# Optimization experiments

Measured on AMD Instinct MI355X. Metric: run time of the kernel, lower is better.

Reference implementation:

```python
import jax, jax.numpy as jnp
import numpy as np

N_NODES = 100000
N_EDGES = 800000
NODE_F = 32
EDGE_F = 16
HID = 128
EPS = 1e-5


def _bn(h, g, b):
    # BatchNorm1d in training mode: biased batch stats over dim 0
    m = h.mean(axis=0)
    v = jnp.mean((h - m) ** 2, axis=0)
    return (h - m) * jax.lax.rsqrt(v + EPS) * g + b


def _sage(x, src, dst, Wl, bl, Wr):
    # PyG SAGEConv (mean aggr): lin_l(mean_{j->i} x_j) + lin_r(x_i)
    s = jax.ops.segment_sum(x[src], dst, num_segments=N_NODES)
    cnt = jax.ops.segment_sum(jnp.ones((src.shape[0], 1), x.dtype), dst, num_segments=N_NODES)
    mean = s / jnp.maximum(cnt, 1.0)
    return mean @ Wl + bl + x @ Wr


def setup_inputs() -> dict:
    key = jax.random.key(0)
    ks = jax.random.split(key, 32)

    def lin(k, fi, fo):
        return jax.random.normal(k, (fi, fo), jnp.float32) / np.sqrt(fi)

    inp = {
        'x': jax.random.normal(ks[0], (N_NODES, NODE_F), jnp.float32),
        'edge_index': jax.random.randint(ks[1], (2, N_EDGES), 0, N_NODES),
        'edge_attr': jax.random.normal(ks[2], (N_EDGES, EDGE_F), jnp.float32),
        'edge_source': jax.random.randint(ks[3], (N_EDGES,), 0, N_NODES),
        'edge_target': jax.random.randint(ks[4], (N_EDGES,), 0, N_NODES),
        'W1l': lin(ks[5], NODE_F, HID), 'b1': jnp.zeros((HID,), jnp.float32), 'W1r': lin(ks[6], NODE_F, HID),
        'W2l': lin(ks[7], HID, HID), 'b2': jnp.zeros((HID,), jnp.float32), 'W2r': lin(ks[8], HID, HID),
        'bn1_g': jnp.ones((HID,), jnp.float32), 'bn1_b': jnp.zeros((HID,), jnp.float32),
        'bn2_g': jnp.ones((HID,), jnp.float32), 'bn2_b': jnp.zeros((HID,), jnp.float32),
        'We': lin(ks[9], EDGE_F, HID), 'be': jnp.zeros((HID,), jnp.float32),
        'bne_g': jnp.ones((HID,), jnp.float32), 'bne_b': jnp.zeros((HID,), jnp.float32),
        'Wm1': lin(ks[10], 3 * HID, HID), 'bm1': jnp.zeros((HID,), jnp.float32),
        'bnm_g': jnp.ones((HID,), jnp.float32), 'bnm_b': jnp.zeros((HID,), jnp.float32),
        'Wm2': lin(ks[11], HID, HID // 2), 'bm2': jnp.zeros((HID // 2,), jnp.float32),
        'Wm3': lin(ks[12], HID // 2, 1), 'bm3': jnp.zeros((1,), jnp.float32),
    }
    return inp


def reference(x, edge_index, edge_attr, edge_source, edge_target,
              W1l, b1, W1r, W2l, b2, W2r, bn1_g, bn1_b, bn2_g, bn2_b,
              We, be, bne_g, bne_b, Wm1, bm1, bnm_g, bnm_b, Wm2, bm2, Wm3, bm3):
    src, dst = edge_index[0], edge_index[1]
    h = jax.nn.relu(_bn(_sage(x, src, dst, W1l, b1, W1r), bn1_g, bn1_b))  # dropout = identity (eval)
    h = jax.nn.relu(_bn(_sage(h, src, dst, W2l, b2, W2r), bn2_g, bn2_b))
    ef = _bn(jax.nn.relu(edge_attr @ We + be), bne_g, bne_b)  # Linear->ReLU->BN->Dropout(id)
    z = jnp.concatenate([h[edge_source], h[edge_target], ef], axis=1)  # [E, 3*HID]
    z = _bn(jax.nn.relu(z @ Wm1 + bm1), bnm_g, bnm_b)
    z = jax.nn.relu(z @ Wm2 + bm2)
    return (z @ Wm3 + bm3).squeeze(-1)
```

## Files before the change

kernel.cpp:

```cpp
#include <hip/hip_runtime.h>
#include <hip/hip_bf16.h>

#define NN 100000
#define NE 800000
#define SCAN_NB 98

typedef __attribute__((ext_vector_type(8))) short bf16x8;
typedef __attribute__((ext_vector_type(4))) float f32x4;

__device__ __forceinline__ short f2b(float f) {
    unsigned u = __float_as_uint(f);
    unsigned r = (u + 0x7fffu + ((u >> 16) & 1u)) >> 16;
    return (short)r;
}
__device__ __forceinline__ float b2f(short s) {
    return __uint_as_float(((unsigned)(unsigned short)s) << 16);
}

__global__ __launch_bounds__(256) void k_hist(const int* __restrict__ ei, int* __restrict__ deg)
{
    int e = blockIdx.x * 256 + threadIdx.x;
    if (e < NE) atomicAdd(&deg[ei[NE + e]], 1);
}

__global__ __launch_bounds__(1024) void k_scan_a(const int* __restrict__ deg,
    int* __restrict__ tmp, int* __restrict__ bsum)
{
    __shared__ int sh[1024];
    int t = threadIdx.x, b = blockIdx.x;
    int idx = b * 1024 + t;
    int v = (idx < NN) ? deg[idx] : 0;
    sh[t] = v;
    __syncthreads();
    for (int ofs = 1; ofs < 1024; ofs <<= 1) {
        int u = (t >= ofs) ? sh[t - ofs] : 0;
        __syncthreads();
        sh[t] += u;
        __syncthreads();
    }
    if (idx < NN) tmp[idx] = sh[t] - v;
    if (t == 1023) bsum[b] = sh[1023];
}

__global__ void k_scan_b(const int* __restrict__ bsum, int* __restrict__ boff,
    int* __restrict__ rowptr)
{
    if (threadIdx.x == 0) {
        int acc = 0;
        for (int i = 0; i < SCAN_NB; i++) { boff[i] = acc; acc += bsum[i]; }
        rowptr[NN] = acc;
    }
}

__global__ __launch_bounds__(1024) void k_scan_c(const int* __restrict__ tmp,
    const int* __restrict__ boff, int* __restrict__ rowptr, int* __restrict__ wp)
{
    int b = blockIdx.x, t = threadIdx.x;
    int idx = b * 1024 + t;
    if (idx < NN) {
        int v = boff[b] + tmp[idx];
        rowptr[idx] = v; wp[idx] = v;
    }
}

__global__ __launch_bounds__(256) void k_scatter(const int* __restrict__ ei,
    int* __restrict__ wp, int* __restrict__ elist)
{
    int e = blockIdx.x * 256 + threadIdx.x;
    if (e < NE) {
        int d = ei[NE + e];
        int pos = atomicAdd(&wp[d], 1);
        elist[pos] = ei[e];
    }
}

__global__ __launch_bounds__(256) void k_gagg1(const float* __restrict__ x,
    const int* __restrict__ rowptr, const int* __restrict__ elist, float* __restrict__ meanX)
{
    int n = blockIdx.x * 8 + (threadIdx.x >> 5);
    int j = threadIdx.x & 31;
    int b = rowptr[n], e = rowptr[n + 1];
    float acc = 0.f;
    for (int i = b; i < e; i++) {
        int s = elist[i];
        acc += x[(size_t)s * 32 + j];
    }
    float inv = (e > b) ? 1.0f / (float)(e - b) : 1.0f;
    meanX[(size_t)n * 32 + j] = acc * inv;
}

__global__ __launch_bounds__(256) void k_gagg2(const short* __restrict__ h1b,
    const int* __restrict__ rowptr, const int* __restrict__ elist,
    const float* __restrict__ sc1, const float* __restrict__ sh1, short* __restrict__ m2b)
{
    int n = blockIdx.x * 8 + (threadIdx.x >> 5);
    int c0 = (threadIdx.x & 31) * 4;
    float sc[4], sh[4];
    #pragma unroll
    for (int i = 0; i < 4; i++) { sc[i] = sc1[c0 + i]; sh[i] = sh1[c0 + i]; }
    int b = rowptr[n], e = rowptr[n + 1];
    float acc[4] = {0.f, 0.f, 0.f, 0.f};
    for (int i = b; i < e; i++) {
        int s = elist[i];
        ushort4 u = *(const ushort4*)(h1b + (size_t)s * 128 + c0);
        acc[0] += fmaxf(b2f((short)u.x) * sc[0] + sh[0], 0.f);
        acc[1] += fmaxf(b2f((short)u.y) * sc[1] + sh[1], 0.f);
        acc[2] += fmaxf(b2f((short)u.z) * sc[2] + sh[2], 0.f);
        acc[3] += fmaxf(b2f((short)u.w) * sc[3] + sh[3], 0.f);
    }
    float inv = (e > b) ? 1.0f / (float)(e - b) : 1.0f;
    ushort4 o;
    o.x = (unsigned short)f2b(acc[0] * inv);
    o.y = (unsigned short)f2b(acc[1] * inv);
    o.z = (unsigned short)f2b(acc[2] * inv);
    o.w = (unsigned short)f2b(acc[3] * inv);
    *(ushort4*)(m2b + (size_t)n * 128 + c0) = o;
}

__global__ __launch_bounds__(256) void k_node_l1(
    const float* __restrict__ meanX, const float* __restrict__ x,
    const float* __restrict__ Wl, const float* __restrict__ Wr,
    const float* __restrict__ bias,
    short* __restrict__ outp, float* __restrict__ ssum, float* __restrict__ ssq)
{
    __shared__ __align__(16) float sWl[32][128];
    __shared__ __align__(16) float sWr[32][128];
    __shared__ __align__(16) float sA[32][36];
    __shared__ __align__(16) float sB[32][36];
    __shared__ float red[2][128], red2[2][128];
    int tid = threadIdx.x;
    int j = tid & 127, rg = tid >> 7;
    int r0 = blockIdx.x * 32;

    for (int f = tid * 4; f < 4096; f += 1024) {
        *(float4*)((float*)sWl + f) = *(const float4*)(Wl + f);
        *(float4*)((float*)sWr + f) = *(const float4*)(Wr + f);
    }
    {
        int r = tid >> 3, c = (tid & 7) * 4;
        *(float4*)(&sA[r][c]) = *(const float4*)(meanX + (size_t)(r0 + r) * 32 + c);
        *(float4*)(&sB[r][c]) = *(const float4*)(x + (size_t)(r0 + r) * 32 + c);
    }
    __syncthreads();

    float acc[16];
    #pragma unroll
    for (int r = 0; r < 16; r++) acc[r] = 0.0f;
    int rb = rg * 16;
    #pragma unroll
    for (int kq = 0; kq < 8; kq++) {
        int k = kq * 4;
        float wl0 = sWl[k][j], wl1 = sWl[k+1][j], wl2 = sWl[k+2][j], wl3 = sWl[k+3][j];
        float wr0 = sWr[k][j], wr1 = sWr[k+1][j], wr2 = sWr[k+2][j], wr3 = sWr[k+3][j];
        #pragma unroll
        for (int r = 0; r < 16; r++) {
            float4 a = *(float4*)(&sA[rb + r][k]);
            float4 b = *(float4*)(&sB[rb + r][k]);
            acc[r] += a.x*wl0 + a.y*wl1 + a.z*wl2 + a.w*wl3
                    + b.x*wr0 + b.y*wr1 + b.z*wr2 + b.w*wr3;
        }
    }
    float bj = bias[j];
    float s1 = 0.0f, s2 = 0.0f;
    #pragma unroll
    for (int r = 0; r < 16; r++) {
        float v = acc[r] + bj;
        outp[(size_t)(r0 + rb + r) * 128 + j] = f2b(v);
        s1 += v; s2 += v * v;
    }
    red[rg][j] = s1; red2[rg][j] = s2;
    __syncthreads();
    if (rg == 0) {
        atomicAdd(&ssum[j], red[0][j] + red[1][j]);
        atomicAdd(&ssq[j],  red2[0][j] + red2[1][j]);
    }
}

__global__ __launch_bounds__(256) void k_node_l2m(
    const short* __restrict__ m2b, const short* __restrict__ h1b,
    const float* __restrict__ sc1, const float* __restrict__ sh1,
    const short* __restrict__ W2cT, const float* __restrict__ bias,
    short* __restrict__ h2b, float* __restrict__ ssum, float* __restrict__ ssq)
{
    __shared__ __align__(16) short sK[32][264];
    __shared__ float sRed[2][128];
    __shared__ float sS[128], sH[128];
    const int tid = threadIdx.x;
    const int wave = tid >> 6, lane = tid & 63, quad = lane >> 4, ln = lane & 15;
    const int waveM = wave >> 1, waveN = wave & 1;
    const int colbase = 64 * waveN, row16 = 16 * waveM;
    if (tid < 128) { sS[tid] = sc1[tid]; sH[tid] = sh1[tid]; sRed[0][tid] = 0.f; sRed[1][tid] = 0.f; }

    bf16x8 bW[4][8];
    #pragma unroll
    for (int nt = 0; nt < 4; nt++)
        #pragma unroll
        for (int kk = 0; kk < 8; kk++)
            bW[nt][kk] = *(const bf16x8*)(W2cT + (size_t)(colbase + nt * 16 + ln) * 256 + kk * 32 + quad * 8);
    float bc[4];
    #pragma unroll
    for (int nt = 0; nt < 4; nt++) bc[nt] = bias[colbase + nt * 16 + ln];

    float s1[4] = {0,0,0,0}, s2[4] = {0,0,0,0};
    f32x4 zero = {0.f, 0.f, 0.f, 0.f};
    __syncthreads();

    for (int t = blockIdx.x; t < NN / 32; t += gridDim.x) {
        int r0 = t * 32;
        __syncthreads();
        {
            int r = tid >> 3, seg = tid & 7;
            if (seg < 4) {
                const bf16x8* src = (const bf16x8*)(m2b + (size_t)(r0 + r) * 128 + seg * 32);
                bf16x8* dst = (bf16x8*)(&sK[r][seg * 32]);
                dst[0] = src[0]; dst[1] = src[1]; dst[2] = src[2]; dst[3] = src[3];
            } else {
                int c0 = (seg - 4) * 32;
                const short* src = h1b + (size_t)(r0 + r) * 128 + c0;
                short tmp[32];
                #pragma unroll
                for (int i = 0; i < 32; i++)
                    tmp[i] = f2b(fmaxf(b2f(src[i]) * sS[c0 + i] + sH[c0 + i], 0.f));
                bf16x8* dst = (bf16x8*)(&sK[r][128 + c0]);
                dst[0] = *(bf16x8*)(tmp); dst[1] = *(bf16x8*)(tmp + 8);
                dst[2] = *(bf16x8*)(tmp + 16); dst[3] = *(bf16x8*)(tmp + 24);
            }
        }
        __syncthreads();
        f32x4 acc[4] = {zero, zero, zero, zero};
        #pragma unroll
        for (int kk = 0; kk < 8; kk++) {
            bf16x8 a = *(const bf16x8*)(&sK[row16 + ln][kk * 32 + quad * 8]);
            #pragma unroll
            for (int nt = 0; nt < 4; nt++)
                acc[nt] = __builtin_amdgcn_mfma_f32_16x16x32_bf16(a, bW[nt][kk], acc[nt], 0, 0, 0);
        }
        #pragma unroll
        for (int nt = 0; nt < 4; nt++) {
            int col = colbase + nt * 16 + ln;
            #pragma unroll
            for (int r = 0; r < 4; r++) {
                float v = acc[nt][r] + bc[nt];
                h2b[(size_t)(r0 + row16 + quad * 4 + r) * 128 + col] = f2b(v);
                s1[nt] += v; s2[nt] += v * v;
            }
        }
    }
    #pragma unroll
    for (int nt = 0; nt < 4; nt++) {
        float a1 = s1[nt], a2 = s2[nt];
        a1 += __shfl_down(a1, 32); a1 += __shfl_down(a1, 16);
        a2 += __shfl_down(a2, 32); a2 += __shfl_down(a2, 16);
        if (quad == 0) {
            atomicAdd(&sRed[0][colbase + nt * 16 + ln], a1);
            atomicAdd(&sRed[1][colbase + nt * 16 + ln], a2);
        }
    }
    __syncthreads();
    if (tid < 128) {
        atomicAdd(&ssum[tid], sRed[0][tid]);
        atomicAdd(&ssq[tid],  sRed[1][tid]);
    }
}

__global__ void k_bn_fin(const float* __restrict__ ssum, const float* __restrict__ ssq,
    const float* __restrict__ g, const float* __restrict__ b, float count,
    float* __restrict__ scale, float* __restrict__ shift)
{
    int j = threadIdx.x;
    float m = ssum[j] / count;
    float var = ssq[j] / count - m * m;
    float rs = rsqrtf(var + 1e-5f);
    float sc = g[j] * rs;
    scale[j] = sc;
    shift[j] = b[j] - m * sc;
}

__global__ void k_prep(const float* __restrict__ We, const float* __restrict__ Wm1,
                       const float* __restrict__ W2l, const float* __restrict__ W2r,
                       short* __restrict__ WteT, short* __restrict__ WmsT,
                       short* __restrict__ WmdT, short* __restrict__ W2cT)
{
    int j = threadIdx.x;
    int b = blockIdx.x;
    if (b == 0) {
        for (int k = 0; k < 32; k++)
            WteT[j * 32 + k] = (k < 16) ? f2b(We[k * 128 + j]) : (short)0;
    } else if (b == 1) {
        for (int k = 0; k < 128; k++) WmsT[j * 128 + k] = f2b(Wm1[k * 128 + j]);
    } else if (b == 2) {
        for (int k = 0; k < 128; k++) WmdT[j * 128 + k] = f2b(Wm1[(128 + k) * 128 + j]);
    } else if (b == 3) {
        for (int k = 0; k < 128; k++) W2cT[j * 256 + k] = f2b(W2l[k * 128 + j]);
    } else {
        for (int k = 0; k < 128; k++) W2cT[j * 256 + 128 + k] = f2b(W2r[k * 128 + j]);
    }
}

__global__ void k_fold_e(const float* __restrict__ ssum, const float* __restrict__ ssq,
    const float* __restrict__ g, const float* __restrict__ b,
    const float* __restrict__ Wm1, const float* __restrict__ bm1,
    short* __restrict__ W1pT, float* __restrict__ bm1p)
{
    __shared__ float sa[128], sc[128];
    int tid = threadIdx.x;
    float m = ssum[tid] / (float)NE;
    float var = ssq[tid] / (float)NE - m * m;
    float rs = rsqrtf(var + 1e-5f);
    float a = g[tid] * rs;
    sa[tid] = a; sc[tid] = b[tid] - m * a;
    __syncthreads();
    float acc = bm1[tid];
    for (int k = 0; k < 128; k++) {
        float w = Wm1[(256 + k) * 128 + tid];
        W1pT[tid * 128 + k] = f2b(sa[k] * w);
        acc += sc[k] * w;
    }
    bm1p[tid] = acc;
}

__global__ void k_fold_m(const float* __restrict__ ssum, const float* __restrict__ ssq,
    const float* __restrict__ g, const float* __restrict__ b,
    const float* __restrict__ Wm2, const float* __restrict__ bm2,
    short* __restrict__ W2pT, float* __restrict__ b2p)
{
    __shared__ float sa[128], sc[128];
    int tid = threadIdx.x;
    float m = ssum[tid] / (float)NE;
    float var = ssq[tid] / (float)NE - m * m;
    float rs = rsqrtf(var + 1e-5f);
    float a = g[tid] * rs;
    sa[tid] = a; sc[tid] = b[tid] - m * a;
    __syncthreads();
    if (tid < 64) {
        float acc = bm2[tid];
        for (int k = 0; k < 128; k++) {
            float w = Wm2[k * 64 + tid];
            W2pT[tid * 128 + k] = f2b(sa[k] * w);
            acc += sc[k] * w;
        }
        b2p[tid] = acc;
    }
}

__global__ __launch_bounds__(256) void k_proj_mfma(
    const short* __restrict__ h2b, const float* __restrict__ sc2, const float* __restrict__ sh2,
    const short* __restrict__ WT, short* __restrict__ C)
{
    __shared__ __align__(16) short sA[32][136];
    __shared__ float sS[128], sH[128];
    const int tid = threadIdx.x;
    const int wave = tid >> 6, lane = tid & 63, quad = lane >> 4, ln = lane & 15;
    const int waveM = wave >> 1, waveN = wave & 1;
    const int colbase = 64 * waveN, row16 = 16 * waveM;
    if (tid < 128) { sS[tid] = sc2[tid]; sH[tid] = sh2[tid]; }
    bf16x8 bW[4][4];
    #pragma unroll
    for (int nt = 0; nt < 4; nt++)
        #pragma unroll
        for (int kk = 0; kk < 4; kk++)
            bW[nt][kk] = *(const bf16x8*)(WT + (colbase + nt * 16 + ln) * 128 + kk * 32 + quad * 8);
    f32x4 zero = {0.f, 0.f, 0.f, 0.f};
    __syncthreads();
    for (int t = blockIdx.x; t < NN / 32; t += gridDim.x) {
        int r0 = t * 32;
        __syncthreads();
        {
            int r = tid >> 3, c0 = (tid & 7) * 16;
            const short* p = h2b + (size_t)(r0 + r) * 128 + c0;
            short tmp[16];
            #pragma unroll
            for (int i = 0; i < 16; i++)
                tmp[i] = f2b(fmaxf(b2f(p[i]) * sS[c0 + i] + sH[c0 + i], 0.f));
            *(bf16x8*)(&sA[r][c0])     = *(bf16x8*)tmp;
            *(bf16x8*)(&sA[r][c0 + 8]) = *(bf16x8*)(tmp + 8);
        }
        __syncthreads();
        f32x4 acc[4] = {zero, zero, zero, zero};
        #pragma unroll
        for (int kk = 0; kk < 4; kk++) {
            bf16x8 a = *(const bf16x8*)(&sA[row16 + ln][kk * 32 + quad * 8]);
            #pragma unroll
            for (int nt = 0; nt < 4; nt++)
                acc[nt] = __builtin_amdgcn_mfma_f32_16x16x32_bf16(a, bW[nt][kk], acc[nt], 0, 0, 0);
        }
        #pragma unroll
        for (int nt = 0; nt < 4; nt++) {
            int col = colbase + nt * 16 + ln;
            #pragma unroll
            for (int r = 0; r < 4; r++)
                C[(size_t)(r0 + row16 + quad * 4 + r) * 128 + col] = f2b(acc[nt][r]);
        }
    }
}

template<int MODE, bool STOREV = false>
__global__ __launch_bounds__(256) void k_edge_mfma(
    const float* __restrict__ ea,
    const short* __restrict__ WteT, const float* __restrict__ be,
    const short* __restrict__ W1pT, const float* __restrict__ bm1p,
    const short* __restrict__ hs, const short* __restrict__ hd,
    const int* __restrict__ esrc, const int* __restrict__ etgt,
    const short* __restrict__ W2pT, const float* __restrict__ b2p,
    const float* __restrict__ Wm3, const float* __restrict__ bm3,
    float* __restrict__ ssum, float* __restrict__ ssq,
    short* __restrict__ vbuf, float* __restrict__ outp)
{
    __shared__ __align__(16) short sT[32][136];
    __shared__ float sRed[2][128];
    __shared__ __align__(16) short sW2[64][136];
    __shared__ float sZ[32][69];
    __shared__ float sW3[64];

    const int tid = threadIdx.x;
    const int wave = tid >> 6, lane = tid & 63;
    const int quad = lane >> 4, ln = lane & 15;
    const int waveM = wave >> 1, waveN = wave & 1;
    const int colbase = 64 * waveN, row16 = 16 * waveM;

    if (MODE < 2) {
        if (tid < 128) { sRed[0][tid] = 0.f; sRed[1][tid] = 0.f; }
    }
    if (MODE >= 2) {
        int q = tid >> 2, kb = (tid & 3) * 32;
        const bf16x8* src = (const bf16x8*)(W2pT + q * 128 + kb);
        bf16x8* dst = (bf16x8*)(&sW2[q][kb]);
        dst[0] = src[0]; dst[1] = src[1]; dst[2] = src[2]; dst[3] = src[3];
        if (tid < 64) sW3[tid] = Wm3[tid];
    }

    bf16x8 bWe[4], bW1[4][4];
    if (MODE <= 2) {
        #pragma unroll
        for (int nt = 0; nt < 4; nt++) {
            bWe[nt] = *(const bf16x8*)(WteT + (colbase + nt * 16 + ln) * 32 + quad * 8);
            if (MODE >= 1) {
                #pragma unroll
                for (int kk = 0; kk < 4; kk++)
                    bW1[nt][kk] = *(const bf16x8*)(W1pT + (colbase + nt * 16 + ln) * 128 + kk * 32 + quad * 8);
            }
        }
    }
    float bec[4], bmc[4];
    #pragma unroll
    for (int nt = 0; nt < 4; nt++) {
        bec[nt] = (MODE <= 2) ? be[colbase + nt * 16 + ln] : 0.f;
        bmc[nt] = (MODE == 1 || MODE == 2) ? bm1p[colbase + nt * 16 + ln] : 0.f;
    }
    float b2c[2] = {0.f, 0.f};
    if (MODE >= 2) { b2c[0] = b2p[32 * waveN + ln]; b2c[1] = b2p[32 * waveN + 16 + ln]; }
    float bm3v = (MODE >= 2) ? bm3[0] : 0.f;

    float s1[4] = {0,0,0,0}, s2[4] = {0,0,0,0};
    f32x4 zero = {0.f, 0.f, 0.f, 0.f};
    __syncthreads();

    for (int t = blockIdx.x; t < NE / 32; t += gridDim.x) {
        const int e0 = t * 32;

        if (MODE == 3) {
            f32x4 vacc[2] = {zero, zero};
            #pragma unroll
            for (int kk = 0; kk < 4; kk++) {
                bf16x8 aV = *(const bf16x8*)(vbuf + (size_t)(e0 + row16 + ln) * 128 + kk * 32 + quad * 8);
                #pragma unroll
                for (int n2 = 0; n2 < 2; n2++) {
                    bf16x8 bV = *(const bf16x8*)(&sW2[32 * waveN + n2 * 16 + ln][kk * 32 + quad * 8]);
                    vacc[n2] = __builtin_amdgcn_mfma_f32_16x16x32_bf16(aV, bV, vacc[n2], 0, 0, 0);
                }
            }
            __syncthreads();
            #pragma unroll
            for (int n2 = 0; n2 < 2; n2++) {
                int col2 = 32 * waveN + n2 * 16 + ln;
                #pragma unroll
                for (int r = 0; r < 4; r++)
                    sZ[row16 + quad * 4 + r][col2] = fmaxf(vacc[n2][r] + b2c[n2], 0.f);
            }
            __syncthreads();
            if (wave == 0) {
                int rw = lane & 31, half = lane >> 5;
                float o = 0.f;
                #pragma unroll 8
                for (int k2 = 0; k2 < 32; k2++)
                    o += sZ[rw][half * 32 + k2] * sW3[half * 32 + k2];
                o += __shfl_down(o, 32);
                if (lane < 32) outp[e0 + rw] = o + bm3v;
            }
            continue;
        }

        bf16x8 aE;
        #pragma unroll
        for (int i = 0; i < 8; i++) aE[i] = 0;
        if (quad < 2) {
            const float* p = ea + (size_t)(e0 + row16 + ln) * 16 + quad * 8;
            float4 f0 = *(const float4*)p, f1 = *(const float4*)(p + 4);
            aE[0]=f2b(f0.x); aE[1]=f2b(f0.y); aE[2]=f2b(f0.z); aE[3]=f2b(f0.w);
            aE[4]=f2b(f1.x); aE[5]=f2b(f1.y); aE[6]=f2b(f1.z); aE[7]=f2b(f1.w);
        }
        f32x4 tacc[4];
        #pragma unroll
        for (int nt = 0; nt < 4; nt++)
            tacc[nt] = __builtin_amdgcn_mfma_f32_16x16x32_bf16(aE, bWe[nt], zero, 0, 0, 0);

        if (MODE == 0) {
            #pragma unroll
            for (int nt = 0; nt < 4; nt++)
                #pragma unroll
                for (int r = 0; r < 4; r++) {
                    float v = fmaxf(tacc[nt][r] + bec[nt], 0.f);
                    s1[nt] += v; s2[nt] += v * v;
                }
            continue;
        }

        __syncthreads();
        #pragma unroll
        for (int nt = 0; nt < 4; nt++) {
            int col = colbase + nt * 16 + ln;
            #pragma unroll
            for (int r = 0; r < 4; r++)
                sT[row16 + quad * 4 + r][col] = f2b(fmaxf(tacc[nt][r] + bec[nt], 0.f));
        }
        __syncthreads();

        f32x4 uacc[4] = {zero, zero, zero, zero};
        #pragma unroll
        for (int kk = 0; kk < 4; kk++) {
            bf16x8 aU = *(const bf16x8*)(&sT[row16 + ln][kk * 32 + quad * 8]);
            #pragma unroll
            for (int nt = 0; nt < 4; nt++)
                uacc[nt] = __builtin_amdgcn_mfma_f32_16x16x32_bf16(aU, bW1[nt][kk], uacc[nt], 0, 0, 0);
        }

        int4 is4 = *(const int4*)(esrc + e0 + row16 + quad * 4);
        int4 it4 = *(const int4*)(etgt + e0 + row16 + quad * 4);
        int isv[4] = {is4.x, is4.y, is4.z, is4.w};
        int itv[4] = {it4.x, it4.y, it4.z, it4.w};

        if (MODE == 1) {
            #pragma unroll
            for (int nt = 0; nt < 4; nt++) {
                int col = colbase + nt * 16 + ln;
                #pragma unroll
                for (int r = 0; r < 4; r++) {
                    float v = uacc[nt][r] + bmc[nt]
                            + b2f(hs[(size_t)isv[r] * 128 + col]) + b2f(hd[(size_t)itv[r] * 128 + col]);
                    v = fmaxf(v, 0.f);
                    s1[nt] += v; s2[nt] += v * v;
                    if constexpr (STOREV)
                        vbuf[(size_t)(e0 + row16 + quad * 4 + r) * 128 + col] = f2b(v);
                }
            }
        } else {
            __syncthreads();
            #pragma unroll
            for (int nt = 0; nt < 4; nt++) {
                int col = colbase + nt * 16 + ln;
                #pragma unroll
                for (int r = 0; r < 4; r++) {
                    float v = uacc[nt][r] + bmc[nt]
                            + b2f(hs[(size_t)isv[r] * 128 + col]) + b2f(hd[(size_t)itv[r] * 128 + col]);
                    sT[row16 + quad * 4 + r][col] = f2b(fmaxf(v, 0.f));
                }
            }
            __syncthreads();
            f32x4 vacc[2] = {zero, zero};
            #pragma unroll
            for (int kk = 0; kk < 4; kk++) {
                bf16x8 aV = *(const bf16x8*)(&sT[row16 + ln][kk * 32 + quad * 8]);
                #pragma unroll
                for (int n2 = 0; n2 < 2; n2++) {
                    bf16x8 bV = *(const bf16x8*)(&sW2[32 * waveN + n2 * 16 + ln][kk * 32 + quad * 8]);
                    vacc[n2] = __builtin_amdgcn_mfma_f32_16x16x32_bf16(aV, bV, vacc[n2], 0, 0, 0);
                }
            }
            #pragma unroll
            for (int n2 = 0; n2 < 2; n2++) {
                int col2 = 32 * waveN + n2 * 16 + ln;
                #pragma unroll
                for (int r = 0; r < 4; r++)
                    sZ[row16 + quad * 4 + r][col2] = fmaxf(vacc[n2][r] + b2c[n2], 0.f);
            }
            __syncthreads();
            if (wave == 0) {
                int rw = lane & 31, half = lane >> 5;
                float o = 0.f;
                #pragma unroll 8
                for (int k2 = 0; k2 < 32; k2++)
                    o += sZ[rw][half * 32 + k2] * sW3[half * 32 + k2];
                o += __shfl_down(o, 32);
                if (lane < 32) outp[e0 + rw] = o + bm3v;
            }
        }
    }

    if (MODE < 2) {
        #pragma unroll
        for (int nt = 0; nt < 4; nt++) {
            float a1 = s1[nt], a2 = s2[nt];
            a1 += __shfl_down(a1, 32); a1 += __shfl_down(a1, 16);
            a2 += __shfl_down(a2, 32); a2 += __shfl_down(a2, 16);
            if (quad == 0) {
                atomicAdd(&sRed[0][colbase + nt * 16 + ln], a1);
                atomicAdd(&sRed[1][colbase + nt * 16 + ln], a2);
            }
        }
        __syncthreads();
        if (tid < 128) {
            atomicAdd(&ssum[tid], sRed[0][tid]);
            atomicAdd(&ssq[tid],  sRed[1][tid]);
        }
    }
}

extern "C" void kernel_launch(void* const* d_in, const int* in_sizes, int n_in,
                              void* d_out, int out_size, void* d_ws, size_t ws_size,
                              hipStream_t stream) {
    const float* x     = (const float*)d_in[0];
    const int*   ei    = (const int*)  d_in[1];
    const float* eattr = (const float*)d_in[2];
    const int*   esrc  = (const int*)  d_in[3];
    const int*   etgt  = (const int*)  d_in[4];
    const float* W1l = (const float*)d_in[5];  const float* b1 = (const float*)d_in[6];
    const float* W1r = (const float*)d_in[7];
    const float* W2l = (const float*)d_in[8];  const float* b2 = (const float*)d_in[9];
    const float* W2r = (const float*)d_in[10];
    const float* bn1_g = (const float*)d_in[11]; const float* bn1_b = (const float*)d_in[12];
    const float* bn2_g = (const float*)d_in[13]; const float* bn2_b = (const float*)d_in[14];
    const float* We  = (const float*)d_in[15]; const float* be  = (const float*)d_in[16];
    const float* bne_g = (const float*)d_in[17]; const float* bne_b = (const float*)d_in[18];
    const float* Wm1 = (const float*)d_in[19]; const float* bm1 = (const float*)d_in[20];
    const float* bnm_g = (const float*)d_in[21]; const float* bnm_b = (const float*)d_in[22];
    const float* Wm2 = (const float*)d_in[23]; const float* bm2 = (const float*)d_in[24];
    const float* Wm3 = (const float*)d_in[25]; const float* bm3 = (const float*)d_in[26];
    float* out = (float*)d_out;

    char* base = (char*)d_ws;
    size_t o = 0;
    auto A = [&](size_t bytes) { char* p = base + o; o = (o + bytes + 255) & ~(size_t)255; return p; };
    short* hsb   = (short*)A((size_t)NN * 128 * 2);
    short* hdb   = (short*)A((size_t)NN * 128 * 2);
    int*   deg   = (int*)  A((size_t)NN * 4);
    int*   rowptr= (int*)  A((size_t)(NN + 1) * 4);
    int*   wp    = (int*)  A((size_t)NN * 4);
    int*   elist = (int*)  A((size_t)NE * 4);
    float* st    = (float*)A(1024 * 4);
    int*   bsum  = (int*)  A(SCAN_NB * 4);
    int*   boff  = (int*)  A(SCAN_NB * 4);
    float* sc1   = (float*)A(512); float* sh1 = (float*)A(512);
    float* sc2   = (float*)A(512); float* sh2 = (float*)A(512);
    float* bm1p  = (float*)A(512); float* b2p = (float*)A(256);
    short* WteT  = (short*)A(128 * 32 * 2);
    short* W1pT  = (short*)A(128 * 128 * 2);
    short* WmsT  = (short*)A(128 * 128 * 2);
    short* WmdT  = (short*)A(128 * 128 * 2);
    short* W2pT  = (short*)A(64 * 128 * 2);
    short* W2cT  = (short*)A(128 * 256 * 2);
    size_t chain = o;
    float* meanX = (float*)A((size_t)NN * 32 * 4);
    short* h1b   = (short*)A((size_t)NN * 128 * 2);
    short* m2b   = (short*)A((size_t)NN * 128 * 2);
    short* h2b   = (short*)A((size_t)NN * 128 * 2);
    int*   stmp  = (int*)meanX;
    short* vbuf  = (short*)(base + chain);
    bool storev = ws_size >= chain + (size_t)NE * 128 * 2;

    hipMemsetAsync(deg, 0, (size_t)NN * 4, stream);
    hipMemsetAsync(st, 0, 1024 * 4, stream);

    k_prep<<<5, 128, 0, stream>>>(We, Wm1, W2l, W2r, WteT, WmsT, WmdT, W2cT);
    k_hist<<<(NE + 255) / 256, 256, 0, stream>>>(ei, deg);
    k_scan_a<<<SCAN_NB, 1024, 0, stream>>>(deg, stmp, bsum);
    k_scan_b<<<1, 64, 0, stream>>>(bsum, boff, rowptr);
    k_scan_c<<<SCAN_NB, 1024, 0, stream>>>(stmp, boff, rowptr, wp);
    k_scatter<<<(NE + 255) / 256, 256, 0, stream>>>(ei, wp, elist);

    k_edge_mfma<0><<<1024, 256, 0, stream>>>(eattr, WteT, be, W1pT, bm1p, hsb, hdb,
        esrc, etgt, W2pT, b2p, Wm3, bm3, st + 512, st + 640, nullptr, out);
    k_fold_e<<<1, 128, 0, stream>>>(st + 512, st + 640, bne_g, bne_b, Wm1, bm1, W1pT, bm1p);

    k_gagg1<<<NN / 8, 256, 0, stream>>>(x, rowptr, elist, meanX);
    k_node_l1<<<NN / 32, 256, 0, stream>>>(meanX, x, W1l, W1r, b1, h1b, st + 0, st + 128);
    k_bn_fin<<<1, 128, 0, stream>>>(st + 0, st + 128, bn1_g, bn1_b, (float)NN, sc1, sh1);

    k_gagg2<<<NN / 8, 256, 0, stream>>>(h1b, rowptr, elist, sc1, sh1, m2b);
    k_node_l2m<<<640, 256, 0, stream>>>(m2b, h1b, sc1, sh1, W2cT, b2, h2b, st + 256, st + 384);
    k_bn_fin<<<1, 128, 0, stream>>>(st + 256, st + 384, bn2_g, bn2_b, (float)NN, sc2, sh2);

    k_proj_mfma<<<640, 256, 0, stream>>>(h2b, sc2, sh2, WmsT, hsb);
    k_proj_mfma<<<640, 256, 0, stream>>>(h2b, sc2, sh2, WmdT, hdb);

    if (storev)
        k_edge_mfma<1, true><<<1280, 256, 0, stream>>>(eattr, WteT, be, W1pT, bm1p, hsb, hdb,
            esrc, etgt, W2pT, b2p, Wm3, bm3, st + 768, st + 896, vbuf, out);
    else
        k_edge_mfma<1, false><<<1280, 256, 0, stream>>>(eattr, WteT, be, W1pT, bm1p, hsb, hdb,
            esrc, etgt, W2pT, b2p, Wm3, bm3, st + 768, st + 896, nullptr, out);
    k_fold_m<<<1, 128, 0, stream>>>(st + 768, st + 896, bnm_g, bnm_b, Wm2, bm2, W2pT, b2p);

    if (storev)
        k_edge_mfma<3><<<2048, 256, 0, stream>>>(eattr, WteT, be, W1pT, bm1p, hsb, hdb,
            esrc, etgt, W2pT, b2p, Wm3, bm3, nullptr, nullptr, vbuf, out);
    else
        k_edge_mfma<2><<<1280, 256, 0, stream>>>(eattr, WteT, be, W1pT, bm1p, hsb, hdb,
            esrc, etgt, W2pT, b2p, Wm3, bm3, nullptr, nullptr, nullptr, out);
}
```

Baseline: 856.6 us.

## Drop edge-activation buffer, recompute with coalesced gathers, bf16 edge attrs, fuse BN finalize

```diff
diff --git a/kernel.cpp b/kernel.cpp
--- a/kernel.cpp
+++ b/kernel.cpp
@@ -91,13 +91,24 @@
 
 __global__ __launch_bounds__(256) void k_gagg2(const short* __restrict__ h1b,
     const int* __restrict__ rowptr, const int* __restrict__ elist,
-    const float* __restrict__ sc1, const float* __restrict__ sh1, short* __restrict__ m2b)
-{
-    int n = blockIdx.x * 8 + (threadIdx.x >> 5);
-    int c0 = (threadIdx.x & 31) * 4;
+    const float* __restrict__ ssum, const float* __restrict__ ssq,
+    const float* __restrict__ g, const float* __restrict__ bb, short* __restrict__ m2b)
+{
+    __shared__ float sS[128], sH[128];
+    int tid = threadIdx.x;
+    if (tid < 128) {
+        float m = ssum[tid] / (float)NN;
+        float var = ssq[tid] / (float)NN - m * m;
+        float rs = rsqrtf(var + 1e-5f);
+        float sc = g[tid] * rs;
+        sS[tid] = sc; sH[tid] = bb[tid] - m * sc;
+    }
+    __syncthreads();
+    int n = blockIdx.x * 8 + (tid >> 5);
+    int c0 = (tid & 31) * 4;
     float sc[4], sh[4];
     #pragma unroll
-    for (int i = 0; i < 4; i++) { sc[i] = sc1[c0 + i]; sh[i] = sh1[c0 + i]; }
+    for (int i = 0; i < 4; i++) { sc[i] = sS[c0 + i]; sh[i] = sH[c0 + i]; }
     int b = rowptr[n], e = rowptr[n + 1];
     float acc[4] = {0.f, 0.f, 0.f, 0.f};
     for (int i = b; i < e; i++) {
@@ -178,7 +189,8 @@
 
 __global__ __launch_bounds__(256) void k_node_l2m(
     const short* __restrict__ m2b, const short* __restrict__ h1b,
-    const float* __restrict__ sc1, const float* __restrict__ sh1,
+    const float* __restrict__ s1sum, const float* __restrict__ s1sq,
+    const float* __restrict__ g1, const float* __restrict__ b1b,
     const short* __restrict__ W2cT, const float* __restrict__ bias,
     short* __restrict__ h2b, float* __restrict__ ssum, float* __restrict__ ssq)
 {
@@ -189,7 +201,14 @@
     const int wave = tid >> 6, lane = tid & 63, quad = lane >> 4, ln = lane & 15;
     const int waveM = wave >> 1, waveN = wave & 1;
     const int colbase = 64 * waveN, row16 = 16 * waveM;
-    if (tid < 128) { sS[tid] = sc1[tid]; sH[tid] = sh1[tid]; sRed[0][tid] = 0.f; sRed[1][tid] = 0.f; }
+    if (tid < 128) {
+        float m = s1sum[tid] / (float)NN;
+        float var = s1sq[tid] / (float)NN - m * m;
+        float rs = rsqrtf(var + 1e-5f);
+        float sc = g1[tid] * rs;
+        sS[tid] = sc; sH[tid] = b1b[tid] - m * sc;
+        sRed[0][tid] = 0.f; sRed[1][tid] = 0.f;
+    }
 
     bf16x8 bW[4][8];
     #pragma unroll
@@ -263,19 +282,6 @@
     }
 }
 
-__global__ void k_bn_fin(const float* __restrict__ ssum, const float* __restrict__ ssq,
-    const float* __restrict__ g, const float* __restrict__ b, float count,
-    float* __restrict__ scale, float* __restrict__ shift)
-{
-    int j = threadIdx.x;
-    float m = ssum[j] / count;
-    float var = ssq[j] / count - m * m;
-    float rs = rsqrtf(var + 1e-5f);
-    float sc = g[j] * rs;
-    scale[j] = sc;
-    shift[j] = b[j] - m * sc;
-}
-
 __global__ void k_prep(const float* __restrict__ We, const float* __restrict__ Wm1,
                        const float* __restrict__ W2l, const float* __restrict__ W2r,
                        short* __restrict__ WteT, short* __restrict__ WmsT,
@@ -343,9 +349,12 @@
     }
 }
 
-__global__ __launch_bounds__(256) void k_proj_mfma(
-    const short* __restrict__ h2b, const float* __restrict__ sc2, const float* __restrict__ sh2,
-    const short* __restrict__ WT, short* __restrict__ C)
+__global__ __launch_bounds__(256) void k_proj2(
+    const short* __restrict__ h2b,
+    const float* __restrict__ s2sum, const float* __restrict__ s2sq,
+    const float* __restrict__ g2, const float* __restrict__ b2b,
+    const short* __restrict__ WsT, const short* __restrict__ WdT,
+    short* __restrict__ Cs, short* __restrict__ Cd)
 {
     __shared__ __align__(16) short sA[32][136];
     __shared__ float sS[128], sH[128];
@@ -353,13 +362,21 @@
     const int wave = tid >> 6, lane = tid & 63, quad = lane >> 4, ln = lane & 15;
     const int waveM = wave >> 1, waveN = wave & 1;
     const int colbase = 64 * waveN, row16 = 16 * waveM;
-    if (tid < 128) { sS[tid] = sc2[tid]; sH[tid] = sh2[tid]; }
-    bf16x8 bW[4][4];
+    if (tid < 128) {
+        float m = s2sum[tid] / (float)NN;
+        float var = s2sq[tid] / (float)NN - m * m;
+        float rs = rsqrtf(var + 1e-5f);
+        float sc = g2[tid] * rs;
+        sS[tid] = sc; sH[tid] = b2b[tid] - m * sc;
+    }
+    bf16x8 bWs[4][4], bWd[4][4];
     #pragma unroll
     for (int nt = 0; nt < 4; nt++)
         #pragma unroll
-        for (int kk = 0; kk < 4; kk++)
-            bW[nt][kk] = *(const bf16x8*)(WT + (colbase + nt * 16 + ln) * 128 + kk * 32 + quad * 8);
+        for (int kk = 0; kk < 4; kk++) {
+            bWs[nt][kk] = *(const bf16x8*)(WsT + (colbase + nt * 16 + ln) * 128 + kk * 32 + quad * 8);
+            bWd[nt][kk] = *(const bf16x8*)(WdT + (colbase + nt * 16 + ln) * 128 + kk * 32 + quad * 8);
+        }
     f32x4 zero = {0.f, 0.f, 0.f, 0.f};
     __syncthreads();
     for (int t = blockIdx.x; t < NN / 32; t += gridDim.x) {
@@ -376,27 +393,33 @@
             *(bf16x8*)(&sA[r][c0 + 8]) = *(bf16x8*)(tmp + 8);
         }
         __syncthreads();
-        f32x4 acc[4] = {zero, zero, zero, zero};
+        f32x4 accS[4] = {zero, zero, zero, zero};
+        f32x4 accD[4] = {zero, zero, zero, zero};
         #pragma unroll
         for (int kk = 0; kk < 4; kk++) {
             bf16x8 a = *(const bf16x8*)(&sA[row16 + ln][kk * 32 + quad * 8]);
             #pragma unroll
-            for (int nt = 0; nt < 4; nt++)
-                acc[nt] = __builtin_amdgcn_mfma_f32_16x16x32_bf16(a, bW[nt][kk], acc[nt], 0, 0, 0);
+            for (int nt = 0; nt < 4; nt++) {
+                accS[nt] = __builtin_amdgcn_mfma_f32_16x16x32_bf16(a, bWs[nt][kk], accS[nt], 0, 0, 0);
+                accD[nt] = __builtin_amdgcn_mfma_f32_16x16x32_bf16(a, bWd[nt][kk], accD[nt], 0, 0, 0);
+            }
         }
         #pragma unroll
         for (int nt = 0; nt < 4; nt++) {
             int col = colbase + nt * 16 + ln;
             #pragma unroll
-            for (int r = 0; r < 4; r++)
-                C[(size_t)(r0 + row16 + quad * 4 + r) * 128 + col] = f2b(acc[nt][r]);
-        }
-    }
-}
-
-template<int MODE, bool STOREV = false>
+            for (int r = 0; r < 4; r++) {
+                size_t idx = (size_t)(r0 + row16 + quad * 4 + r) * 128 + col;
+                Cs[idx] = f2b(accS[nt][r]);
+                Cd[idx] = f2b(accD[nt][r]);
+            }
+        }
+    }
+}
+
+template<int MODE>
 __global__ __launch_bounds__(256) void k_edge_mfma(
-    const float* __restrict__ ea,
+    const float* __restrict__ ea, short* __restrict__ ea_bf,
     const short* __restrict__ WteT, const float* __restrict__ be,
     const short* __restrict__ W1pT, const float* __restrict__ bm1p,
     const short* __restrict__ hs, const short* __restrict__ hd,
@@ -404,10 +427,11 @@
     const short* __restrict__ W2pT, const float* __restrict__ b2p,
     const float* __restrict__ Wm3, const float* __restrict__ bm3,
     float* __restrict__ ssum, float* __restrict__ ssq,
-    short* __restrict__ vbuf, float* __restrict__ outp)
+    float* __restrict__ outp)
 {
     __shared__ __align__(16) short sT[32][136];
     __shared__ float sRed[2][128];
+    __shared__ __align__(16) float sG[32][132];
     __shared__ __align__(16) short sW2[64][136];
     __shared__ float sZ[32][69];
     __shared__ float sW3[64];
@@ -421,7 +445,7 @@
     if (MODE < 2) {
         if (tid < 128) { sRed[0][tid] = 0.f; sRed[1][tid] = 0.f; }
     }
-    if (MODE >= 2) {
+    if (MODE == 2) {
         int q = tid >> 2, kb = (tid & 3) * 32;
         const bf16x8* src = (const bf16x8*)(W2pT + q * 128 + kb);
         bf16x8* dst = (bf16x8*)(&sW2[q][kb]);
@@ -430,26 +454,26 @@
     }
 
     bf16x8 bWe[4], bW1[4][4];
-    if (MODE <= 2) {
-        #pragma unroll
-        for (int nt = 0; nt < 4; nt++) {
-            bWe[nt] = *(const bf16x8*)(WteT + (colbase + nt * 16 + ln) * 32 + quad * 8);
-            if (MODE >= 1) {
-                #pragma unroll
-                for (int kk = 0; kk < 4; kk++)
-                    bW1[nt][kk] = *(const bf16x8*)(W1pT + (colbase + nt * 16 + ln) * 128 + kk * 32 + quad * 8);
-            }
+    #pragma unroll
+    for (int nt = 0; nt < 4; nt++) {
+        bWe[nt] = *(const bf16x8*)(WteT + (colbase + nt * 16 + ln) * 32 + quad * 8);
+        if (MODE >= 1) {
+            #pragma unroll
+            for (int kk = 0; kk < 4; kk++)
+                bW1[nt][kk] = *(const bf16x8*)(W1pT + (colbase + nt * 16 + ln) * 128 + kk * 32 + quad * 8);
         }
     }
     float bec[4], bmc[4];
     #pragma unroll
     for (int nt = 0; nt < 4; nt++) {
-        bec[nt] = (MODE <= 2) ? be[colbase + nt * 16 + ln] : 0.f;
-        bmc[nt] = (MODE == 1 || MODE == 2) ? bm1p[colbase + nt * 16 + ln] : 0.f;
+        bec[nt] = be[colbase + nt * 16 + ln];
+        bmc[nt] = (MODE >= 1) ? bm1p[colbase + nt * 16 + ln] : 0.f;
     }
     float b2c[2] = {0.f, 0.f};
-    if (MODE >= 2) { b2c[0] = b2p[32 * waveN + ln]; b2c[1] = b2p[32 * waveN + 16 + ln]; }
-    float bm3v = (MODE >= 2) ? bm3[0] : 0.f;
+    if (MODE == 2) { b2c[0] = b2p[32 * waveN + ln]; b2c[1] = b2p[32 * waveN + 16 + ln]; }
+    float bm3v = (MODE == 2) ? bm3[0] : 0.f;
+
+    const int g_er = tid >> 3, g_cb = (tid & 7) * 16;
 
     float s1[4] = {0,0,0,0}, s2[4] = {0,0,0,0};
     f32x4 zero = {0.f, 0.f, 0.f, 0.f};
@@ -458,51 +482,35 @@
     for (int t = blockIdx.x; t < NE / 32; t += gridDim.x) {
         const int e0 = t * 32;
 
-        if (MODE == 3) {
-            f32x4 vacc[2] = {zero, zero};
-            #pragma unroll
-            for (int kk = 0; kk < 4; kk++) {
-                bf16x8 aV = *(const bf16x8*)(vbuf + (size_t)(e0 + row16 + ln) * 128 + kk * 32 + quad * 8);
-                #pragma unroll
-                for (int n2 = 0; n2 < 2; n2++) {
-                    bf16x8 bV = *(const bf16x8*)(&sW2[32 * waveN + n2 * 16 + ln][kk * 32 + quad * 8]);
-                    vacc[n2] = __builtin_amdgcn_mfma_f32_16x16x32_bf16(aV, bV, vacc[n2], 0, 0, 0);
-                }
-            }
-            __syncthreads();
-            #pragma unroll
-            for (int n2 = 0; n2 < 2; n2++) {
-                int col2 = 32 * waveN + n2 * 16 + ln;
-                #pragma unroll
-                for (int r = 0; r < 4; r++)
-                    sZ[row16 + quad * 4 + r][col2] = fmaxf(vacc[n2][r] + b2c[n2], 0.f);
-            }
-            __syncthreads();
-            if (wave == 0) {
-                int rw = lane & 31, half = lane >> 5;
-                float o = 0.f;
-                #pragma unroll 8
-                for (int k2 = 0; k2 < 32; k2++)
-                    o += sZ[rw][half * 32 + k2] * sW3[half * 32 + k2];
-                o += __shfl_down(o, 32);
-                if (lane < 32) outp[e0 + rw] = o + bm3v;
-            }
-            continue;
+        bf16x8 ga0, ga1, gb0, gb1;
+        if (MODE >= 1) {
+            int es_ = esrc[e0 + g_er], et_ = etgt[e0 + g_er];
+            const short* ps = hs + (size_t)es_ * 128 + g_cb;
+            const short* pd = hd + (size_t)et_ * 128 + g_cb;
+            ga0 = *(const bf16x8*)ps;      ga1 = *(const bf16x8*)(ps + 8);
+            gb0 = *(const bf16x8*)pd;      gb1 = *(const bf16x8*)(pd + 8);
         }
 
         bf16x8 aE;
         #pragma unroll
         for (int i = 0; i < 8; i++) aE[i] = 0;
-        if (quad < 2) {
-            const float* p = ea + (size_t)(e0 + row16 + ln) * 16 + quad * 8;
-            float4 f0 = *(const float4*)p, f1 = *(const float4*)(p + 4);
-            aE[0]=f2b(f0.x); aE[1]=f2b(f0.y); aE[2]=f2b(f0.z); aE[3]=f2b(f0.w);
-            aE[4]=f2b(f1.x); aE[5]=f2b(f1.y); aE[6]=f2b(f1.z); aE[7]=f2b(f1.w);
+        if (MODE == 0) {
+            if (quad < 2) {
+                const float* p = ea + (size_t)(e0 + row16 + ln) * 16 + quad * 8;
+                float4 f0 = *(const float4*)p, f1 = *(const float4*)(p + 4);
+                aE[0]=f2b(f0.x); aE[1]=f2b(f0.y); aE[2]=f2b(f0.z); aE[3]=f2b(f0.w);
+                aE[4]=f2b(f1.x); aE[5]=f2b(f1.y); aE[6]=f2b(f1.z); aE[7]=f2b(f1.w);
+                if (waveN == 0)
+                    *(bf16x8*)(ea_bf + (size_t)(e0 + row16 + ln) * 16 + quad * 8) = aE;
+            }
+        } else {
+            if (quad < 2)
+                aE = *(const bf16x8*)(ea_bf + (size_t)(e0 + row16 + ln) * 16 + quad * 8);
         }
         f32x4 tacc[4];
         #pragma unroll
         for (int nt = 0; nt < 4; nt++)
-            tacc[nt] = __builtin_amdgcn_mfma_f32_16x16x32_bf16(aE, bWe[nt], zero, 0, 0, 0);
+            tacc[nt] = __builtin_amdgcn_mfma_f32_16x16x32_bf16(aE, bWe[nt], tacc[nt] = zero, 0, 0, 0);
 
         if (MODE == 0) {
             #pragma unroll
@@ -523,6 +531,17 @@
             for (int r = 0; r < 4; r++)
                 sT[row16 + quad * 4 + r][col] = f2b(fmaxf(tacc[nt][r] + bec[nt], 0.f));
         }
+        {
+            float tf[16];
+            #pragma unroll
+            for (int i = 0; i < 8; i++) {
+                tf[i]     = b2f(ga0[i]) + b2f(gb0[i]);
+                tf[8 + i] = b2f(ga1[i]) + b2f(gb1[i]);
+            }
+            #pragma unroll
+            for (int q4 = 0; q4 < 4; q4++)
+                *(float4*)(&sG[g_er][g_cb + q4 * 4]) = *(float4*)(tf + q4 * 4);
+        }
         __syncthreads();
 
         f32x4 uacc[4] = {zero, zero, zero, zero};
@@ -533,11 +552,6 @@
             for (int nt = 0; nt < 4; nt++)
                 uacc[nt] = __builtin_amdgcn_mfma_f32_16x16x32_bf16(aU, bW1[nt][kk], uacc[nt], 0, 0, 0);
         }
-
-        int4 is4 = *(const int4*)(esrc + e0 + row16 + quad * 4);
-        int4 it4 = *(const int4*)(etgt + e0 + row16 + quad * 4);
-        int isv[4] = {is4.x, is4.y, is4.z, is4.w};
-        int itv[4] = {it4.x, it4.y, it4.z, it4.w};
 
         if (MODE == 1) {
             #pragma unroll
@@ -545,12 +559,9 @@
                 int col = colbase + nt * 16 + ln;
                 #pragma unroll
                 for (int r = 0; r < 4; r++) {
-                    float v = uacc[nt][r] + bmc[nt]
-                            + b2f(hs[(size_t)isv[r] * 128 + col]) + b2f(hd[(size_t)itv[r] * 128 + col]);
+                    float v = uacc[nt][r] + bmc[nt] + sG[row16 + quad * 4 + r][col];
                     v = fmaxf(v, 0.f);
                     s1[nt] += v; s2[nt] += v * v;
-                    if constexpr (STOREV)
-                        vbuf[(size_t)(e0 + row16 + quad * 4 + r) * 128 + col] = f2b(v);
                 }
             }
         } else {
@@ -560,8 +571,7 @@
                 int col = colbase + nt * 16 + ln;
                 #pragma unroll
                 for (int r = 0; r < 4; r++) {
-                    float v = uacc[nt][r] + bmc[nt]
-                            + b2f(hs[(size_t)isv[r] * 128 + col]) + b2f(hd[(size_t)itv[r] * 128 + col]);
+                    float v = uacc[nt][r] + bmc[nt] + sG[row16 + quad * 4 + r][col];
                     sT[row16 + quad * 4 + r][col] = f2b(fmaxf(v, 0.f));
                 }
             }
@@ -642,6 +652,7 @@
     auto A = [&](size_t bytes) { char* p = base + o; o = (o + bytes + 255) & ~(size_t)255; return p; };
     short* hsb   = (short*)A((size_t)NN * 128 * 2);
     short* hdb   = (short*)A((size_t)NN * 128 * 2);
+    short* ea_bf = (short*)A((size_t)NE * 16 * 2);
     int*   deg   = (int*)  A((size_t)NN * 4);
     int*   rowptr= (int*)  A((size_t)(NN + 1) * 4);
     int*   wp    = (int*)  A((size_t)NN * 4);
@@ -649,8 +660,6 @@
     float* st    = (float*)A(1024 * 4);
     int*   bsum  = (int*)  A(SCAN_NB * 4);
     int*   boff  = (int*)  A(SCAN_NB * 4);
-    float* sc1   = (float*)A(512); float* sh1 = (float*)A(512);
-    float* sc2   = (float*)A(512); float* sh2 = (float*)A(512);
     float* bm1p  = (float*)A(512); float* b2p = (float*)A(256);
     short* WteT  = (short*)A(128 * 32 * 2);
     short* W1pT  = (short*)A(128 * 128 * 2);
@@ -658,14 +667,11 @@
     short* WmdT  = (short*)A(128 * 128 * 2);
     short* W2pT  = (short*)A(64 * 128 * 2);
     short* W2cT  = (short*)A(128 * 256 * 2);
-    size_t chain = o;
     float* meanX = (float*)A((size_t)NN * 32 * 4);
     short* h1b   = (short*)A((size_t)NN * 128 * 2);
     short* m2b   = (short*)A((size_t)NN * 128 * 2);
     short* h2b   = (short*)A((size_t)NN * 128 * 2);
     int*   stmp  = (int*)meanX;
-    short* vbuf  = (short*)(base + chain);
-    bool storev = ws_size >= chain + (size_t)NE * 128 * 2;
 
     hipMemsetAsync(deg, 0, (size_t)NN * 4, stream);
     hipMemsetAsync(st, 0, 1024 * 4, stream);
@@ -677,33 +683,23 @@
     k_scan_c<<<SCAN_NB, 1024, 0, stream>>>(stmp, boff, rowptr, wp);
     k_scatter<<<(NE + 255) / 256, 256, 0, stream>>>(ei, wp, elist);
 
-    k_edge_mfma<0><<<1024, 256, 0, stream>>>(eattr, WteT, be, W1pT, bm1p, hsb, hdb,
-        esrc, etgt, W2pT, b2p, Wm3, bm3, st + 512, st + 640, nullptr, out);
+    k_edge_mfma<0><<<1024, 256, 0, stream>>>(eattr, ea_bf, WteT, be, W1pT, bm1p, hsb, hdb,
+        esrc, etgt, W2pT, b2p, Wm3, bm3, st + 512, st + 640, out);
     k_fold_e<<<1, 128, 0, stream>>>(st + 512, st + 640, bne_g, bne_b, Wm1, bm1, W1pT, bm1p);
 
     k_gagg1<<<NN / 8, 256, 0, stream>>>(x, rowptr, elist, meanX);
     k_node_l1<<<NN / 32, 256, 0, stream>>>(meanX, x, W1l, W1r, b1, h1b, st + 0, st + 128);
-    k_bn_fin<<<1, 128, 0, stream>>>(st + 0, st + 128, bn1_g, bn1_b, (float)NN, sc1, sh1);
-
-    k_gagg2<<<NN / 8, 256, 0, stream>>>(h1b, rowptr, elist, sc1, sh1, m2b);
-    k_node_l2m<<<640, 256, 0, stream>>>(m2b, h1b, sc1, sh1, W2cT, b2, h2b, st + 256, st + 384);
-    k_bn_fin<<<1, 128, 0, stream>>>(st + 256, st + 384, bn2_g, bn2_b, (float)NN, sc2, sh2);
-
-    k_proj_mfma<<<640, 256, 0, stream>>>(h2b, sc2, sh2, WmsT, hsb);
-    k_proj_mfma<<<640, 256, 0, stream>>>(h2b, sc2, sh2, WmdT, hdb);
-
-    if (storev)
-        k_edge_mfma<1, true><<<1280, 256, 0, stream>>>(eattr, WteT, be, W1pT, bm1p, hsb, hdb,
-            esrc, etgt, W2pT, b2p, Wm3, bm3, st + 768, st + 896, vbuf, out);
-    else
-        k_edge_mfma<1, false><<<1280, 256, 0, stream>>>(eattr, WteT, be, W1pT, bm1p, hsb, hdb,
-            esrc, etgt, W2pT, b2p, Wm3, bm3, st + 768, st + 896, nullptr, out);
+
+    k_gagg2<<<NN / 8, 256, 0, stream>>>(h1b, rowptr, elist, st + 0, st + 128, bn1_g, bn1_b, m2b);
+    k_node_l2m<<<640, 256, 0, stream>>>(m2b, h1b, st + 0, st + 128, bn1_g, bn1_b,
+                                        W2cT, b2, h2b, st + 256, st + 384);
+
+    k_proj2<<<640, 256, 0, stream>>>(h2b, st + 256, st + 384, bn2_g, bn2_b, WmsT, WmdT, hsb, hdb);
+
+    k_edge_mfma<1><<<2048, 256, 0, stream>>>(eattr, ea_bf, WteT, be, W1pT, bm1p, hsb, hdb,
+        esrc, etgt, W2pT, b2p, Wm3, bm3, st + 768, st + 896, out);
     k_fold_m<<<1, 128, 0, stream>>>(st + 768, st + 896, bnm_g, bnm_b, Wm2, bm2, W2pT, b2p);
 
-    if (storev)
-        k_edge_mfma<3><<<2048, 256, 0, stream>>>(eattr, WteT, be, W1pT, bm1p, hsb, hdb,
-            esrc, etgt, W2pT, b2p, Wm3, bm3, nullptr, nullptr, vbuf, out);
-    else
-        k_edge_mfma<2><<<1280, 256, 0, stream>>>(eattr, WteT, be, W1pT, bm1p, hsb, hdb,
-            esrc, etgt, W2pT, b2p, Wm3, bm3, nullptr, nullptr, nullptr, out);
-}
+    k_edge_mfma<2><<<2048, 256, 0, stream>>>(eattr, ea_bf, WteT, be, W1pT, bm1p, hsb, hdb,
+        esrc, etgt, W2pT, b2p, Wm3, bm3, nullptr, nullptr, out);
+}
```

Measured after the change: 876.7 us. +2.4%, slower.
